# Kernel tuning notes

Hardware: AMD Instinct MI355X
Metric: run time of the kernel (lower is better)

The kernel has to match this reference:

```python
import jax, jax.numpy as jnp
import numpy as np

B, N, D = 8, 2048, 512


def setup_inputs() -> dict:
    key = jax.random.key(0)
    ks = jax.random.split(key, 16)
    s = 1.0 / np.sqrt(D)  # ~ torch Linear default init scale
    inp = {
        "X": jax.random.normal(ks[0], (B, N, D), jnp.float32),
        "Y": jax.random.normal(ks[1], (B, N, D), jnp.float32),
    }
    names = ["xq", "xk", "xv", "yq", "yk", "yv"]
    for i, nm in enumerate(names):
        inp[f"W_{nm}"] = jax.random.uniform(ks[2 + 2 * i], (D, D), jnp.float32, -s, s)
        inp[f"b_{nm}"] = jax.random.uniform(ks[3 + 2 * i], (D,), jnp.float32, -s, s)
    return inp


def _lin(x, W, b):
    # torch nn.Linear: x @ W^T + b
    return jnp.einsum("bnd,ed->bne", x, W) + b


def reference(X, Y, W_xq, b_xq, W_xk, b_xk, W_xv, b_xv, W_yq, b_yq, W_yk, b_yk, W_yv, b_yv):
    d = X.shape[-1]
    scale = 1.0 / jnp.sqrt(jnp.asarray(d, X.dtype))
    Q1, K1, V1 = _lin(X, W_xq, b_xq), _lin(X, W_xk, b_xk), _lin(X, W_xv, b_xv)
    Q2, K2, V2 = _lin(Y, W_yq, b_yq), _lin(Y, W_yk, b_yk), _lin(Y, W_yv, b_yv)
    # NOTE: F.softmax called without dim on a 3-D tensor -> torch legacy dim=0 (batch axis).
    S1 = jnp.einsum("bnd,bmd->bnm", Q1, K2) * scale  # [B, N, N]
    A1 = jax.nn.softmax(S1, axis=0)
    U_A1 = X + jnp.einsum("bnm,bmd->bnd", A1, V2)  # dropout = identity (eval)
    S2 = jnp.einsum("bnd,bmd->bnm", Q2, K1) * scale
    A2 = jax.nn.softmax(S2, axis=0)
    U_A2 = Y + jnp.einsum("bnm,bmd->bnd", A2, V1)
    return U_A1 + U_A2
```

## Files before the change

### kernel.cpp

```cpp
#include <hip/hip_runtime.h>

typedef unsigned short u16;
typedef unsigned char u8;
typedef __attribute__((ext_vector_type(8))) short bf16x8;
typedef __attribute__((ext_vector_type(4))) float f32x4;
typedef __attribute__((ext_vector_type(8))) u16 u16x8;
typedef __attribute__((ext_vector_type(2))) int i32x2;
typedef __attribute__((ext_vector_type(2))) float f32x2;

#define GLOAD_LDS(g, s) __builtin_amdgcn_global_load_lds( \
    (const __attribute__((address_space(1))) void*)(g),   \
    (__attribute__((address_space(3))) void*)(s), 16, 0, 0)

__device__ __forceinline__ u16 f2bf(float f) {
  union { float f; unsigned u; } v; v.f = f;
  unsigned r = v.u + 0x7fffu + ((v.u >> 16) & 1u);
  return (u16)(r >> 16);
}
__device__ __forceinline__ float bf2f(u16 h) {
  union { unsigned u; float f; } v; v.u = ((unsigned)h) << 16;
  return v.f;
}

__device__ __forceinline__ unsigned lds_addr(const void* p) {
  return (unsigned)(unsigned long long)(__attribute__((address_space(3))) const void*)p;
}
__device__ __forceinline__ bf16x8 ds128(const void* p) {
  bf16x8 r;
  asm volatile("ds_read_b128 %0, %1" : "=v"(r) : "v"(lds_addr(p)));
  return r;
}
__device__ __forceinline__ i32x2 ds64(const void* p) {
  i32x2 r;
  asm volatile("ds_read_b64 %0, %1" : "=v"(r) : "v"(lds_addr(p)));
  return r;
}
__device__ __forceinline__ bf16x8 cvt8(i32x2 v) {
  f32x2 f0 = __builtin_amdgcn_cvt_pk_f32_fp8(v[0], false);
  f32x2 f1 = __builtin_amdgcn_cvt_pk_f32_fp8(v[0], true);
  f32x2 f2 = __builtin_amdgcn_cvt_pk_f32_fp8(v[1], false);
  f32x2 f3 = __builtin_amdgcn_cvt_pk_f32_fp8(v[1], true);
  unsigned w0, w1, w2, w3;
  asm("v_cvt_pk_bf16_f32 %0, %1, %2" : "=v"(w0) : "v"(f0[0]), "v"(f0[1]));
  asm("v_cvt_pk_bf16_f32 %0, %1, %2" : "=v"(w1) : "v"(f1[0]), "v"(f1[1]));
  asm("v_cvt_pk_bf16_f32 %0, %1, %2" : "=v"(w2) : "v"(f2[0]), "v"(f2[1]));
  asm("v_cvt_pk_bf16_f32 %0, %1, %2" : "=v"(w3) : "v"(f3[0]), "v"(f3[1]));
  union { unsigned w[4]; bf16x8 v8; } u;
  u.w[0] = w0; u.w[1] = w1; u.w[2] = w2; u.w[3] = w3;
  return u.v8;
}

__device__ __forceinline__ void stage_pair(const u16* gA, int lda, const u16* gB, int ldb,
                                           u16* lA, u16* lB, int wave, int lane) {
  int row = (wave << 4) + (lane >> 2);
  int kb  = (lane & 3) << 3;
  GLOAD_LDS(gA + row * lda + kb,        lA + (wave << 9));
  GLOAD_LDS(gA + (row + 64) * lda + kb, lA + ((wave + 4) << 9));
  GLOAD_LDS(gB + row * ldb + kb,        lB + (wave << 9));
  GLOAD_LDS(gB + (row + 64) * ldb + kb, lB + ((wave + 4) << 9));
}

__device__ __forceinline__ void gemm_seg(f32x4 (&acc)[4][4],
    const u16* Ag, const u16* Bg, int lda, int ldb, int nk,
    u16* As, u16* Bs, int wave, int lane) {
  const int wr = (wave >> 1) << 6, wc = (wave & 1) << 6;
  const int rl = lane & 15, rk = (lane >> 4) << 3;
  stage_pair(Ag, lda, Bg, ldb, As, Bs, wave, lane);
  if (nk > 1)
    stage_pair(Ag + 32, lda, Bg + 32, ldb, As + 4096, Bs + 4096, wave, lane);
  int bufsel = 0;
  for (int kt = 0; kt < nk; ++kt) {
    if (kt + 1 < nk) asm volatile("s_waitcnt vmcnt(4)" ::: "memory");
    else             asm volatile("s_waitcnt vmcnt(0)" ::: "memory");
    __builtin_amdgcn_s_barrier();
    asm volatile("" ::: "memory");
    if (kt + 2 < nk) {
      int nb = bufsel + 2; if (nb >= 3) nb -= 3;
      stage_pair(Ag + (long)(kt + 2) * 32, lda, Bg + (long)(kt + 2) * 32, ldb,
                 As + nb * 4096, Bs + nb * 4096, wave, lane);
    }
    const u16* ab = As + bufsel * 4096;
    const u16* bb = Bs + bufsel * 4096;
    bf16x8 af[4], bfr[4];
#pragma unroll
    for (int i = 0; i < 4; i++)
      af[i]  = *(const bf16x8*)(ab + ((wr + (i << 4) + rl) << 5) + rk);
#pragma unroll
    for (int j = 0; j < 4; j++)
      bfr[j] = *(const bf16x8*)(bb + ((wc + (j << 4) + rl) << 5) + rk);
#pragma unroll
    for (int i = 0; i < 4; i++)
#pragma unroll
      for (int j = 0; j < 4; j++)
        acc[i][j] = __builtin_amdgcn_mfma_f32_16x16x32_bf16(af[i], bfr[j], acc[i][j], 0, 0, 0);
    __builtin_amdgcn_sched_barrier(0);
    bufsel = bufsel + 1; if (bufsel == 3) bufsel = 0;
  }
}

__device__ __forceinline__ void stage_one(const u16* g, int ld, u16* d, int tid) {
  int rw = tid >> 3;
  int gs = ((tid & 7) ^ (rw & 7)) << 3;
  int wb = (tid >> 6) << 9;
#pragma unroll
  for (int p = 0; p < 4; p++)
    GLOAD_LDS(g + (long)(p * 64 + rw) * ld + gs, d + p * 4096 + wb);
}

__device__ __forceinline__ void gemm256d(f32x4 (&acc)[8][4],
    const u16* Ag, int lda, const u16* Bg, int ldb, int nk,
    u16* As, u16* Bs, int tid) {
  const int lane = tid & 63, wid = tid >> 6;
  const int wr = (wid >> 2) << 7;
  const int wc = (wid & 3) << 6;
  const int rl = lane & 15, kg = lane >> 4;
  const int swz0 = (kg ^ (rl & 7)) << 3;
  const int rbA = (wr + rl) * 64, rbB = (wc + rl) * 64;

  stage_one(Ag, lda, As, tid);
  stage_one(Bg, ldb, Bs, tid);
  if (nk > 1) stage_one(Ag + 64, lda, As + 16384, tid);

  int ba = 0;
  for (int t = 0; t < nk; ++t) {
    if (t + 1 < nk) asm volatile("s_waitcnt vmcnt(4)" ::: "memory");
    else            asm volatile("s_waitcnt vmcnt(0)" ::: "memory");
    __builtin_amdgcn_s_barrier();
    if (t + 1 < nk)
      stage_one(Bg + (t + 1) * 64, ldb, Bs + ((t + 1) & 1) * 16384, tid);
    if (t + 2 < nk) {
      int nb = ba + 2; if (nb >= 3) nb -= 3;
      stage_one(Ag + (long)(t + 2) * 64, lda, As + nb * 16384, tid);
    }
    const u16* ab = As + ba * 16384 + rbA;
    const u16* bb = Bs + (t & 1) * 16384 + rbB;
#pragma unroll
    for (int kk = 0; kk < 2; kk++) {
      const int sw = swz0 ^ (kk << 5);
      bf16x8 a[8], b[4];
#pragma unroll
      for (int i = 0; i < 8; i++) a[i] = ds128(ab + i * 1024 + sw);
#pragma unroll
      for (int j = 0; j < 4; j++) b[j] = ds128(bb + j * 1024 + sw);
      asm volatile("s_waitcnt lgkmcnt(0)" ::: "memory");
      __builtin_amdgcn_sched_barrier(0);
      __builtin_amdgcn_s_setprio(1);
#pragma unroll
      for (int i = 0; i < 8; i++)
#pragma unroll
        for (int j = 0; j < 4; j++)
          acc[i][j] = __builtin_amdgcn_mfma_f32_16x16x32_bf16(a[i], b[j], acc[i][j], 0, 0, 0);
      __builtin_amdgcn_s_setprio(0);
      __builtin_amdgcn_sched_barrier(0);
    }
    ba = ba + 1; if (ba == 3) ba = 0;
  }
}

__device__ __forceinline__ void stage_A64(const u8* gA, u8* Ad, int tid) {
#pragma unroll
  for (int pass = 0; pass < 2; pass++) {
    int gid = pass * 512 + tid;
    int row = gid >> 2, g = gid & 3;
    GLOAD_LDS(gA + (long)row * 2048 + ((g ^ (row & 3)) << 4), Ad + (gid << 4));
  }
}
__device__ __forceinline__ void stage_B64(const u16* gB, u8* Bd, int tid) {
#pragma unroll
  for (int pass = 0; pass < 2; pass++) {
    int gid = pass * 512 + tid;
    int row = gid >> 3, g = gid & 7;
    GLOAD_LDS(gB + (long)row * 2048 + ((g ^ (row & 7)) << 3), Bd + (gid << 4));
  }
}

__device__ __forceinline__ void gemm_pv8(f32x4 (&acc)[4][4],
    const u8* Ag, const u16* Bg, u8* As, u8* Bs, int tid) {
  const int lane = tid & 63, wid = tid >> 6;
  const int mq = wid >> 1, nh = wid & 1;
  const int rl = lane & 15, kg = lane >> 4;
  const int nk = 16;
  const int abase = (mq * 64 + rl) * 64 + ((kg & 1) << 3);
  const int bbase = (nh * 64 + rl) * 128;

  stage_A64(Ag, As, tid);
  stage_B64(Bg, Bs, tid);
  stage_A64(Ag + 64, As + 16384, tid);
  int ba = 0;
  for (int t = 0; t < nk; ++t) {
    if (t + 1 < nk) asm volatile("s_waitcnt vmcnt(2)" ::: "memory");
    else            asm volatile("s_waitcnt vmcnt(0)" ::: "memory");
    __builtin_amdgcn_s_barrier();
    if (t + 1 < nk) stage_B64(Bg + (t + 1) * 64, Bs + ((t + 1) & 1) * 16384, tid);
    if (t + 2 < nk) {
      int nb = ba + 2; if (nb >= 3) nb -= 3;
      stage_A64(Ag + (long)(t + 2) * 64, As + nb * 16384, tid);
    }
    const u8* ab = As + ba * 16384 + abase;
    const u8* bb = Bs + (t & 1) * 16384 + bbase;
#pragma unroll
    for (int kk = 0; kk < 2; kk++) {
      const int sa = (((kk << 1) + (kg >> 1)) ^ (rl & 3)) << 4;
      const int sb = (((kk << 2) + kg) ^ (rl & 7)) << 4;
      i32x2 ar[4]; bf16x8 bfr[4];
#pragma unroll
      for (int i = 0; i < 4; i++) ar[i] = ds64(ab + i * 1024 + sa);
#pragma unroll
      for (int j = 0; j < 4; j++) bfr[j] = ds128(bb + j * 2048 + sb);
      asm volatile("s_waitcnt lgkmcnt(0)" ::: "memory");
      __builtin_amdgcn_sched_barrier(0);
      bf16x8 a[4];
#pragma unroll
      for (int i = 0; i < 4; i++) a[i] = cvt8(ar[i]);
      __builtin_amdgcn_s_setprio(1);
#pragma unroll
      for (int i = 0; i < 4; i++)
#pragma unroll
        for (int j = 0; j < 4; j++)
          acc[i][j] = __builtin_amdgcn_mfma_f32_16x16x32_bf16(a[i], bfr[j], acc[i][j], 0, 0, 0);
      __builtin_amdgcn_s_setprio(0);
      __builtin_amdgcn_sched_barrier(0);
    }
    ba = ba + 1; if (ba == 3) ba = 0;
  }
}

__global__ __launch_bounds__(256) void k_cvt2(const float* __restrict__ inX,
                                              const float* __restrict__ inY,
                                              u16* __restrict__ oX, u16* __restrict__ oY,
                                              int n8) {
  int i = blockIdx.x * 256 + threadIdx.x;
  const float* in = (i < n8) ? inX : inY;
  u16* out = (i < n8) ? oX : oY;
  int k = (i < n8) ? i : i - n8;
  const float4* pf = (const float4*)in + (long)k * 2;
  float4 a = pf[0], b = pf[1];
  u16x8 o;
  o[0] = f2bf(a.x); o[1] = f2bf(a.y); o[2] = f2bf(a.z); o[3] = f2bf(a.w);
  o[4] = f2bf(b.x); o[5] = f2bf(b.y); o[6] = f2bf(b.z); o[7] = f2bf(b.w);
  *((u16x8*)out + k) = o;
}

struct P6 { const float* p[6]; };
struct O6 { u16* p[6]; };

__global__ __launch_bounds__(256) void k_cvt_w(P6 w, u16* __restrict__ out) {
  int z = blockIdx.y;
  int i = blockIdx.x * 256 + threadIdx.x;
  const float4* pf = (const float4*)w.p[z] + (long)i * 2;
  float4 a = pf[0], b = pf[1];
  u16x8 o;
  o[0] = f2bf(a.x); o[1] = f2bf(a.y); o[2] = f2bf(a.z); o[3] = f2bf(a.w);
  o[4] = f2bf(b.x); o[5] = f2bf(b.y); o[6] = f2bf(b.z); o[7] = f2bf(b.w);
  *((u16x8*)(out + (long)z * 262144) + i) = o;
}

__global__ __launch_bounds__(256) void k_proj(const u16* __restrict__ Xb, const u16* __restrict__ Yb,
                                              const u16* __restrict__ Wb, P6 bias, O6 dst) {
  __shared__ u16 As[12288], Bs[12288];
  int x = blockIdx.x;
  int swz = (x & 7) * 384 + (x >> 3);
  int bm = swz / 24;
  int r  = swz - bm * 24;
  int z = r >> 2, bn = r & 3;
  int tid = threadIdx.x, wave = tid >> 6, lane = tid & 63;
  const u16* Ag = (z < 3 ? Xb : Yb) + (long)bm * 128 * 512;
  const u16* Bg = Wb + (long)z * 262144 + (long)bn * 128 * 512;
  f32x4 acc[4][4] = {};
  gemm_seg(acc, Ag, Bg, 512, 512, 16, As, Bs, wave, lane);
  const float* bi = bias.p[z];
  u16* D = dst.p[z];
  int wr = (wave >> 1) << 6, wc = (wave & 1) << 6;
  int row0 = bm * 128 + wr + ((lane >> 4) << 2);
  int col0 = bn * 128 + wc + (lane & 15);
  float bj[4];
#pragma unroll
  for (int j = 0; j < 4; j++) bj[j] = bi[col0 + (j << 4)];
#pragma unroll
  for (int i = 0; i < 4; i++)
#pragma unroll
    for (int j = 0; j < 4; j++)
#pragma unroll
      for (int rr = 0; rr < 4; rr++)
        D[(long)(row0 + (i << 4) + rr) * 512 + col0 + (j << 4)] = f2bf(acc[i][j][rr] + bj[j]);
}

__global__ __launch_bounds__(512) void k_s(const u16* __restrict__ Q, const u16* __restrict__ K,
                                           u16* __restrict__ S) {
  __shared__ u16 As[49152], Bs[32768];
  int x = blockIdx.x;
  int swz = (x & 7) * 64 + (x >> 3);
  int bn = swz & 7, bm = (swz >> 3) & 7, b = swz >> 6;
  int tid = threadIdx.x;
  const u16* Ag = Q + (long)b * 1048576 + (long)bm * 256 * 512;
  const u16* Bg = K + (long)b * 1048576 + (long)bn * 256 * 512;
  f32x4 acc[8][4] = {};
  gemm256d(acc, Ag, 512, Bg, 512, 8, As, Bs, tid);
  u16* D = S + (long)b * 4194304;
  const float scale = 0.04419417382415922f;
  int lane = tid & 63, wid = tid >> 6;
  int row0 = bm * 256 + ((wid >> 2) << 7) + ((lane >> 4) << 2);
  int col0 = bn * 256 + ((wid & 3) << 6) + (lane & 15);
#pragma unroll
  for (int i = 0; i < 8; i++)
#pragma unroll
    for (int j = 0; j < 4; j++)
#pragma unroll
      for (int rr = 0; rr < 4; rr++)
        D[(long)(row0 + (i << 4) + rr) * 2048 + col0 + (j << 4)] = f2bf(acc[i][j][rr] * scale);
}

__global__ __launch_bounds__(256) void k_softmax8(const u16* __restrict__ S,
                                                  u8* __restrict__ A8) {
  int idx = blockIdx.x * 256 + threadIdx.x;
  u16x8 v[8];
#pragma unroll
  for (int b = 0; b < 8; b++) v[b] = *((const u16x8*)(S + (long)b * 4194304) + idx);
  unsigned w0[8], w1[8];
#pragma unroll
  for (int jp = 0; jp < 4; jp++) {
    float va[8], vb[8];
    {
      float e[8], m = -1e30f;
#pragma unroll
      for (int b = 0; b < 8; b++) { e[b] = bf2f(v[b][2 * jp]); m = fmaxf(m, e[b]); }
      float s = 0.f;
#pragma unroll
      for (int b = 0; b < 8; b++) { e[b] = __expf(e[b] - m); s += e[b]; }
      float inv = 1.0f / s;
#pragma unroll
      for (int b = 0; b < 8; b++) va[b] = e[b] * inv;
    }
    {
      float e[8], m = -1e30f;
#pragma unroll
      for (int b = 0; b < 8; b++) { e[b] = bf2f(v[b][2 * jp + 1]); m = fmaxf(m, e[b]); }
      float s = 0.f;
#pragma unroll
      for (int b = 0; b < 8; b++) { e[b] = __expf(e[b] - m); s += e[b]; }
      float inv = 1.0f / s;
#pragma unroll
      for (int b = 0; b < 8; b++) vb[b] = e[b] * inv;
    }
#pragma unroll
    for (int b = 0; b < 8; b++) {
      if (jp == 0)      w0[b] = __builtin_amdgcn_cvt_pk_fp8_f32(va[b], vb[b], 0,     false);
      else if (jp == 1) w0[b] = __builtin_amdgcn_cvt_pk_fp8_f32(va[b], vb[b], w0[b], true);
      else if (jp == 2) w1[b] = __builtin_amdgcn_cvt_pk_fp8_f32(va[b], vb[b], 0,     false);
      else              w1[b] = __builtin_amdgcn_cvt_pk_fp8_f32(va[b], vb[b], w1[b], true);
    }
  }
#pragma unroll
  for (int b = 0; b < 8; b++) {
    i32x2 w; w[0] = (int)w0[b]; w[1] = (int)w1[b];
    *(i32x2*)(A8 + (long)b * 4194304 + (long)idx * 8) = w;
  }
}

__global__ __launch_bounds__(256) void k_tr(const u16* __restrict__ V1, const u16* __restrict__ V2,
                                            u16* __restrict__ T1, u16* __restrict__ T2) {
  __shared__ u16 tile[64][65];
  int z = blockIdx.z;
  const u16* src = (z < 8 ? V1 : V2) + (long)(z & 7) * 1048576;
  u16*       dst = (z < 8 ? T1 : T2) + (long)(z & 7) * 1048576;
  int n0 = blockIdx.x * 64, d0 = blockIdx.y * 64;
  int t = threadIdx.x;
  int r = t >> 2, cs = (t & 3) * 16;
  const u16x8* sp = (const u16x8*)(src + (long)(n0 + r) * 512 + d0 + cs);
  u16x8 a = sp[0], b = sp[1];
#pragma unroll
  for (int jj = 0; jj < 8; jj++) { tile[r][cs + jj] = a[jj]; tile[r][cs + 8 + jj] = b[jj]; }
  __syncthreads();
  u16x8 o0, o1;
#pragma unroll
  for (int jj = 0; jj < 8; jj++) { o0[jj] = tile[cs + jj][r]; o1[jj] = tile[cs + 8 + jj][r]; }
  u16x8* op = (u16x8*)(dst + (long)(d0 + r) * 2048 + n0 + cs);
  op[0] = o0; op[1] = o1;
}

__global__ __launch_bounds__(512) void k_pv8m(const u8* __restrict__ A2, const u16* __restrict__ Vt1,
                                              const u8* __restrict__ A1, const u16* __restrict__ Vt2,
                                              const float* __restrict__ X, const float* __restrict__ Y,
                                              float* __restrict__ out, float* __restrict__ P) {
  __shared__ u8 As[49152], Bs[32768];
  int x = blockIdx.x;
  int swz = (x & 7) * 64 + (x >> 3);
  int b = swz >> 6;
  int r = swz & 63;
  int bn = r & 3, kc = (r >> 2) & 1, bm = r >> 3;
  int tid = threadIdx.x;
  long aoff = (long)b * 4194304 + (long)bm * 256 * 2048 + kc * 1024;
  long voff = (long)b * 1048576 + (long)bn * 128 * 2048 + kc * 1024;
  f32x4 acc[4][4] = {};
  gemm_pv8(acc, A2 + aoff, Vt1 + voff, As, Bs, tid);
  __builtin_amdgcn_s_barrier();
  gemm_pv8(acc, A1 + aoff, Vt2 + voff, As, Bs, tid);
  int lane = tid & 63, wid = tid >> 6;
  int mq = wid >> 1, nh = wid & 1;
  int row0 = bm * 256 + mq * 64 + ((lane >> 4) << 2);
  int col0 = bn * 128 + nh * 64 + (lane & 15);
  long base = (long)b * 1048576;
#pragma unroll
  for (int i = 0; i < 4; i++)
#pragma unroll
    for (int j = 0; j < 4; j++)
#pragma unroll
      for (int rr = 0; rr < 4; rr++) {
        long idx = base + (long)(row0 + (i << 4) + rr) * 512 + col0 + (j << 4);
        float v = acc[i][j][rr];
        if (kc) P[idx] = v;
        else    out[idx] = v + X[idx] + Y[idx];
      }
}

__global__ __launch_bounds__(256) void k_fin(float* __restrict__ out, const float* __restrict__ P) {
  long i = (long)(blockIdx.x * 256 + threadIdx.x) * 4;
  float4 o = *(const float4*)(out + i);
  float4 p = *(const float4*)(P + i);
  o.x += p.x; o.y += p.y; o.z += p.z; o.w += p.w;
  *(float4*)(out + i) = o;
}

extern "C" void kernel_launch(void* const* d_in, const int* in_sizes, int n_in,
                              void* d_out, int out_size, void* d_ws, size_t ws_size,
                              hipStream_t stream) {
  const float* X = (const float*)d_in[0];
  const float* Y = (const float*)d_in[1];
  P6 wp, bp;
  for (int i = 0; i < 6; i++) { wp.p[i] = (const float*)d_in[2 + 2 * i]; bp.p[i] = (const float*)d_in[3 + 2 * i]; }

  const long NX = 8L * 2048 * 512;
  const long NS = 8L * 2048 * 2048;
  u16* p = (u16*)d_ws;
  u16* Xb = p;  p += NX;
  u16* Yb = p;  p += NX;
  u16* Wb = p;  p += 6L * 512 * 512;
  u16* Q1 = p;  p += NX;
  u16* K2 = p;  p += NX;
  u16* Q2 = p;  p += NX;
  u16* K1 = p;  p += NX;
  u16* Sb = p;  p += NS;
  u16* V1 = Sb;
  u16* V2 = Sb + NX;
  u16* Vt1 = Xb;
  u16* Vt2 = Yb;
  u8* A8_2 = (u8*)Q2;
  u8* A8_1 = (u8*)Q1;
  float* Pbuf = (float*)Sb;
  (void)ws_size; (void)in_sizes; (void)n_in; (void)out_size;

  dim3 T(256);
  k_cvt2<<<dim3(8192), T, 0, stream>>>(X, Y, Xb, Yb, (int)(NX / 8));
  k_cvt_w<<<dim3(128, 6), T, 0, stream>>>(wp, Wb);
  O6 dst; dst.p[0] = Q1; dst.p[1] = K1; dst.p[2] = V1; dst.p[3] = Q2; dst.p[4] = K2; dst.p[5] = V2;
  k_proj<<<dim3(3072), T, 0, stream>>>(Xb, Yb, Wb, bp, dst);
  k_tr<<<dim3(32, 8, 16), T, 0, stream>>>(V1, V2, Vt1, Vt2);
  k_s<<<dim3(512), dim3(512), 0, stream>>>(Q2, K1, Sb);
  k_softmax8<<<dim3(2048), T, 0, stream>>>(Sb, A8_2);
  k_s<<<dim3(512), dim3(512), 0, stream>>>(Q1, K2, Sb);
  k_softmax8<<<dim3(2048), T, 0, stream>>>(Sb, A8_1);
  k_pv8m<<<dim3(512), dim3(512), 0, stream>>>(A8_2, Vt1, A8_1, Vt2, X, Y, (float*)d_out, Pbuf);
  k_fin<<<dim3((int)(NX / 1024)), T, 0, stream>>>((float*)d_out, Pbuf);
}
```

Measured before the change: 343.0 us.

## Load fp8 attention operand directly into registers instead of staging through LDS

The PV GEMM now loads the fp8 A operand (softmax probabilities) straight from global memory into registers, double-buffered two k-steps ahead, rather than staging it in LDS with global_load_lds. The V operand stays in LDS but moves to a triple buffer, and the A LDS allocation is dropped. This removes the LDS traffic and ds_read instructions for A and shrinks shared memory use. In exchange it adds register pressure and uncoalesced 8-byte global loads, since A is reused by only two waves in the block.

```diff
diff --git a/kernel.cpp b/kernel.cpp
--- a/kernel.cpp
+++ b/kernel.cpp
@@ -28,11 +28,6 @@
 __device__ __forceinline__ bf16x8 ds128(const void* p) {
   bf16x8 r;
   asm volatile("ds_read_b128 %0, %1" : "=v"(r) : "v"(lds_addr(p)));
-  return r;
-}
-__device__ __forceinline__ i32x2 ds64(const void* p) {
-  i32x2 r;
-  asm volatile("ds_read_b64 %0, %1" : "=v"(r) : "v"(lds_addr(p)));
   return r;
 }
 __device__ __forceinline__ bf16x8 cvt8(i32x2 v) {
@@ -157,14 +152,6 @@
   }
 }
 
-__device__ __forceinline__ void stage_A64(const u8* gA, u8* Ad, int tid) {
-#pragma unroll
-  for (int pass = 0; pass < 2; pass++) {
-    int gid = pass * 512 + tid;
-    int row = gid >> 2, g = gid & 3;
-    GLOAD_LDS(gA + (long)row * 2048 + ((g ^ (row & 3)) << 4), Ad + (gid << 4));
-  }
-}
 __device__ __forceinline__ void stage_B64(const u16* gB, u8* Bd, int tid) {
 #pragma unroll
   for (int pass = 0; pass < 2; pass++) {
@@ -174,44 +161,53 @@
   }
 }
 
-__device__ __forceinline__ void gemm_pv8(f32x4 (&acc)[4][4],
-    const u8* Ag, const u16* Bg, u8* As, u8* Bs, int tid) {
+__device__ __forceinline__ void loadA8(const u8* At, i32x2 (&r)[2][4],
+                                       int mq, int rl, int kg) {
+  const u8* base = At + (long)(mq * 64 + rl) * 2048 + (kg << 3);
+#pragma unroll
+  for (int kk = 0; kk < 2; kk++)
+#pragma unroll
+    for (int i = 0; i < 4; i++)
+      r[kk][i] = *(const i32x2*)(base + (long)i * 32768 + (kk << 5));
+}
+
+__device__ __forceinline__ void gemm_pv_reg(f32x4 (&acc)[4][4],
+    const u8* Ag, const u16* Bg, u8* Bs, int tid) {
   const int lane = tid & 63, wid = tid >> 6;
   const int mq = wid >> 1, nh = wid & 1;
   const int rl = lane & 15, kg = lane >> 4;
-  const int nk = 16;
-  const int abase = (mq * 64 + rl) * 64 + ((kg & 1) << 3);
   const int bbase = (nh * 64 + rl) * 128;
-
-  stage_A64(Ag, As, tid);
+  i32x2 ar[2][2][4];
+
   stage_B64(Bg, Bs, tid);
-  stage_A64(Ag + 64, As + 16384, tid);
-  int ba = 0;
-  for (int t = 0; t < nk; ++t) {
-    if (t + 1 < nk) asm volatile("s_waitcnt vmcnt(2)" ::: "memory");
+  asm volatile("" ::: "memory");
+  loadA8(Ag, ar[0], mq, rl, kg);
+  asm volatile("" ::: "memory");
+  stage_B64(Bg + 64, Bs + 16384, tid);
+  asm volatile("" ::: "memory");
+  loadA8(Ag + 64, ar[1], mq, rl, kg);
+  asm volatile("" ::: "memory");
+#pragma unroll
+  for (int t = 0; t < 16; ++t) {
+    if (t + 1 < 16) asm volatile("s_waitcnt vmcnt(10)" ::: "memory");
     else            asm volatile("s_waitcnt vmcnt(0)" ::: "memory");
     __builtin_amdgcn_s_barrier();
-    if (t + 1 < nk) stage_B64(Bg + (t + 1) * 64, Bs + ((t + 1) & 1) * 16384, tid);
-    if (t + 2 < nk) {
-      int nb = ba + 2; if (nb >= 3) nb -= 3;
-      stage_A64(Ag + (long)(t + 2) * 64, As + nb * 16384, tid);
-    }
-    const u8* ab = As + ba * 16384 + abase;
-    const u8* bb = Bs + (t & 1) * 16384 + bbase;
+    if (t + 2 < 16) {
+      stage_B64(Bg + (t + 2) * 64, Bs + ((t + 2) % 3) * 16384, tid);
+      asm volatile("" ::: "memory");
+    }
+    const u8* bb = Bs + (t % 3) * 16384 + bbase;
 #pragma unroll
     for (int kk = 0; kk < 2; kk++) {
-      const int sa = (((kk << 1) + (kg >> 1)) ^ (rl & 3)) << 4;
       const int sb = (((kk << 2) + kg) ^ (rl & 7)) << 4;
-      i32x2 ar[4]; bf16x8 bfr[4];
-#pragma unroll
-      for (int i = 0; i < 4; i++) ar[i] = ds64(ab + i * 1024 + sa);
+      bf16x8 bfr[4];
 #pragma unroll
       for (int j = 0; j < 4; j++) bfr[j] = ds128(bb + j * 2048 + sb);
       asm volatile("s_waitcnt lgkmcnt(0)" ::: "memory");
       __builtin_amdgcn_sched_barrier(0);
       bf16x8 a[4];
 #pragma unroll
-      for (int i = 0; i < 4; i++) a[i] = cvt8(ar[i]);
+      for (int i = 0; i < 4; i++) a[i] = cvt8(ar[t & 1][kk][i]);
       __builtin_amdgcn_s_setprio(1);
 #pragma unroll
       for (int i = 0; i < 4; i++)
@@ -221,7 +217,10 @@
       __builtin_amdgcn_s_setprio(0);
       __builtin_amdgcn_sched_barrier(0);
     }
-    ba = ba + 1; if (ba == 3) ba = 0;
+    if (t + 2 < 16) {
+      loadA8(Ag + (t + 2) * 64, ar[t & 1], mq, rl, kg);
+      asm volatile("" ::: "memory");
+    }
   }
 }
 
@@ -382,7 +381,7 @@
                                               const u8* __restrict__ A1, const u16* __restrict__ Vt2,
                                               const float* __restrict__ X, const float* __restrict__ Y,
                                               float* __restrict__ out, float* __restrict__ P) {
-  __shared__ u8 As[49152], Bs[32768];
+  __shared__ u8 Bs[49152];
   int x = blockIdx.x;
   int swz = (x & 7) * 64 + (x >> 3);
   int b = swz >> 6;
@@ -392,9 +391,9 @@
   long aoff = (long)b * 4194304 + (long)bm * 256 * 2048 + kc * 1024;
   long voff = (long)b * 1048576 + (long)bn * 128 * 2048 + kc * 1024;
   f32x4 acc[4][4] = {};
-  gemm_pv8(acc, A2 + aoff, Vt1 + voff, As, Bs, tid);
+  gemm_pv_reg(acc, A2 + aoff, Vt1 + voff, Bs, tid);
   __builtin_amdgcn_s_barrier();
-  gemm_pv8(acc, A1 + aoff, Vt2 + voff, As, Bs, tid);
+  gemm_pv_reg(acc, A1 + aoff, Vt2 + voff, Bs, tid);
   int lane = tid & 63, wid = tid >> 6;
   int mq = wid >> 1, nh = wid & 1;
   int row0 = bm * 256 + mq * 64 + ((lane >> 4) << 2);
```

New measurement: 422.2 us. 1.23x slower.
